# Optimization experiments

Hardware: AMD Instinct MI355X
Metric: run time of the kernel (lower is better)

Reference implementation:

```python
import jax, jax.numpy as jnp
import numpy as np

ALPHA = 1.0
K = 5          # kernel height == width
STRIDE = 1


def extract_patches(x, k, stride):
    """x: (N, C, H, W) -> (N, k*k*C, Ho, Wo), feature order (kh, kw, c)
    to match k.view(kh*kw*C, F) flattening of a (kh, kw, C, F) kernel."""
    p = jax.lax.conv_general_dilated_patches(x, (k, k), (stride, stride), 'VALID')
    N, _, Ho, Wo = p.shape
    C = x.shape[1]
    # conv_general_dilated_patches is channel-major: (C, kh, kw) -> reorder to (kh, kw, C)
    p = p.reshape(N, C, k, k, Ho, Wo).transpose(0, 2, 3, 1, 4, 5)
    return p.reshape(N, k * k * C, Ho, Wo)


def setup_inputs():
    key = jax.random.key(0)
    kx, kk1, kk2 = jax.random.split(key, 3)
    N, C, H, W = 8, 4, 64, 64
    F = 16
    # xavier-uniform-ish scale for kernels
    limit = float(np.sqrt(6.0 / (K * K * C + F)))
    x = jax.random.normal(kx, (N, C, H, W), jnp.float32)
    k1 = jax.random.uniform(kk1, (K, K, C, F), jnp.float32, -limit, limit)
    k2 = jax.random.uniform(kk2, (K, K, C, F), jnp.float32, -limit, limit)
    bias = jnp.zeros((F,), jnp.float32)
    return {"x": x, "k1": k1, "k2": k2, "bias": bias}


def _smooth_max(patches, kflat):
    # patches: (N, P, Ho, Wo); kflat: (P, F)
    z = patches[:, :, None] + kflat[None, :, :, None, None]  # (N, P, F, Ho, Wo)
    w = jax.nn.softmax(ALPHA * z, axis=1)  # exp(alpha*z)/sum over patch dim (stable)
    return jnp.sum(z * w, axis=1)          # (N, F, Ho, Wo)


def reference(x, k1, k2, bias):
    kh, kw, C, F = k1.shape
    patches = extract_patches(x, kh, STRIDE)        # (N, kh*kw*C, Ho, Wo)
    y11 = _smooth_max(patches, k1.reshape(-1, F))   # smooth-max of  x + k1
    y21 = _smooth_max(-patches, k2.reshape(-1, F))  # smooth-max of -x + k2
    return y11 + y21 + bias[None, :, None, None]
```

## Files before the change

### kernel.cpp

```cpp
#include <hip/hip_runtime.h>

#define NN 8
#define CC 4
#define HH 64
#define WW 64
#define KK 5
#define FF 16
#define HO 60
#define WO 60
#define PP (KK * KK * CC)

typedef float v4f __attribute__((ext_vector_type(4)));

#define PQ_ELEMS (CC * KK * 64)
#define LDS_TOT 1536

__global__ void smorph_weights(const float* __restrict__ k1,
                               const float* __restrict__ k2,
                               float* __restrict__ wq) {
    int i = blockIdx.x * blockDim.x + threadIdx.x;
    if (i < 4 * PP * 16) {
        int idx16 = i >> 4;
        int ff = idx16 / PP;
        int p = idx16 - ff * PP;
        int j = i & 15;
        int grp = j >> 2;
        int fi = j & 3;
        int f = ff * 4 + fi;
        const float* kp = (grp >> 1) ? k2 : k1;
        float kv = kp[p * FF + f];
        float e = __expf(kv);
        wq[i] = (grp & 1) ? kv * e : e;
    }
}

__global__ __launch_bounds__(512) void smorph_conv(
        const float* __restrict__ x, const float* __restrict__ wq,
        const float* __restrict__ bias, float* __restrict__ out) {
    __shared__ v4f lds[LDS_TOT];
    v4f* pq = lds;

    int b = blockIdx.x;
    int n = b / (HO * 2);
    int rem = b - n * (HO * 2);
    int ho = rem >> 1;
    int fgh = rem & 1;
    int t = threadIdx.x;

    for (int i = t; i < PQ_ELEMS; i += 512) {
        int w = i & 63;
        int cr = i >> 6;
        int c = cr / KK, r = cr - c * KK;
        float v = x[((n * CC + c) * HH + (ho + r)) * WW + w];
        float e1 = __expf(v), e2 = __expf(-v);
        pq[i] = (v4f){e1, v * e1, e2, -v * e2};
    }
    __syncthreads();

    int lane = t & 63;
    int wid = t >> 6;
    int cw = wid & 3;
    int fgl = wid >> 2;

    int wbi = __builtin_amdgcn_readfirstlane(((fgh * 2 + fgl) * PP + cw) * 16);
    const float* wb = wq + wbi;

    float d1[4] = {0.f, 0.f, 0.f, 0.f}, n1[4] = {0.f, 0.f, 0.f, 0.f};
    float d2[4] = {0.f, 0.f, 0.f, 0.f}, n2[4] = {0.f, 0.f, 0.f, 0.f};

    const v4f* pbase = pq + (cw * KK) * 64 + lane;

#pragma unroll 1
    for (int kh = 0; kh < KK; ++kh) {
        const v4f* prow = pbase + kh * 64;
        v4f q[KK];
#pragma unroll
        for (int kw = 0; kw < KK; ++kw) q[kw] = prow[kw];
#pragma unroll
        for (int kw = 0; kw < KK; ++kw) {
            const float* wp = wb + (kh * KK + kw) * (CC * 16);
            v4f qv = q[kw];
#pragma unroll
            for (int j = 0; j < 4; ++j) {
                float ea1 = wp[j], ba1 = wp[4 + j];
                float ea2 = wp[8 + j], bb2 = wp[12 + j];
                d1[j] = fmaf(qv.x, ea1, d1[j]);
                n1[j] = fmaf(qv.y, ea1, n1[j]);
                n1[j] = fmaf(qv.x, ba1, n1[j]);
                d2[j] = fmaf(qv.z, ea2, d2[j]);
                n2[j] = fmaf(qv.w, ea2, n2[j]);
                n2[j] = fmaf(qv.z, bb2, n2[j]);
            }
        }
    }

    v4f* red = lds;
    __syncthreads();
    if (cw) {
        v4f* rr = red + (((cw - 1) * 2 + fgl) * 4) * 64 + lane;
        rr[0 * 64] = (v4f){d1[0], d1[1], d1[2], d1[3]};
        rr[1 * 64] = (v4f){n1[0], n1[1], n1[2], n1[3]};
        rr[2 * 64] = (v4f){d2[0], d2[1], d2[2], d2[3]};
        rr[3 * 64] = (v4f){n2[0], n2[1], n2[2], n2[3]};
    }
    __syncthreads();
    if (!cw && lane < WO) {
#pragma unroll
        for (int rcw = 0; rcw < 3; ++rcw) {
            const v4f* rr = red + ((rcw * 2 + fgl) * 4) * 64 + lane;
            v4f t0 = rr[0 * 64], t1 = rr[1 * 64];
            v4f t2 = rr[2 * 64], t3 = rr[3 * 64];
#pragma unroll
            for (int j = 0; j < 4; ++j) {
                d1[j] += t0[j]; n1[j] += t1[j];
                d2[j] += t2[j]; n2[j] += t3[j];
            }
        }
        int f0 = (fgh * 2 + fgl) * 4;
#pragma unroll
        for (int j = 0; j < 4; ++j) {
            float o = n1[j] / d1[j] + n2[j] / d2[j] + bias[f0 + j];
            out[((size_t)(n * FF + f0 + j) * HO + ho) * WO + lane] = o;
        }
    }
}

extern "C" void kernel_launch(void* const* d_in, const int* in_sizes, int n_in,
                              void* d_out, int out_size, void* d_ws, size_t ws_size,
                              hipStream_t stream) {
    const float* x    = (const float*)d_in[0];
    const float* k1   = (const float*)d_in[1];
    const float* k2   = (const float*)d_in[2];
    const float* bias = (const float*)d_in[3];
    float* out = (float*)d_out;
    float* wq = (float*)d_ws;

    smorph_weights<<<(4 * PP * 16 + 255) / 256, 256, 0, stream>>>(k1, k2, wq);
    smorph_conv<<<NN * HO * 2, 512, 0, stream>>>(x, wq, bias, out);
}
```

Before: 70.90 us.

## Compute two output rows per block with 2 filters per wave, reusing weight registers

Each block now handles two output rows and a quarter of the filters (2 per wave) instead of one row and half the filters. Weights are reordered so each wave loads 40 contiguous scalars per kernel row into registers and reuses them for both output rows. Input rows are carried across kh iterations in registers (sliding window). The goal is fewer redundant weight loads and less repeated exp work on shared input rows per output; the cost is more registers per thread and an unchanged block count (8*30*4 = 960).

```diff
diff --git a/kernel.cpp b/kernel.cpp
--- a/kernel.cpp
+++ b/kernel.cpp
@@ -10,23 +10,28 @@
 #define WO 60
 #define PP (KK * KK * CC)
 
+#define RPB 2
+#define HPB (HO / RPB)
+#define RIN (RPB + KK - 1)
+
 typedef float v4f __attribute__((ext_vector_type(4)));
 
-#define PQ_ELEMS (CC * KK * 64)
-#define LDS_TOT 1536
+#define PQ_ELEMS (CC * RIN * 64)
+#define LDS_TOT (PQ_ELEMS + 4)
 
 __global__ void smorph_weights(const float* __restrict__ k1,
                                const float* __restrict__ k2,
                                float* __restrict__ wq) {
     int i = blockIdx.x * blockDim.x + threadIdx.x;
-    if (i < 4 * PP * 16) {
-        int idx16 = i >> 4;
-        int ff = idx16 / PP;
-        int p = idx16 - ff * PP;
-        int j = i & 15;
-        int grp = j >> 2;
-        int fi = j & 3;
-        int f = ff * 4 + fi;
+    if (i < 6400) {
+        int rec = i >> 3, j = i & 7;
+        int cfp = rec / 25, khkw = rec - cfp * 25;
+        int kh = khkw / 5, kw = khkw - kh * 5;
+        int fqfp = cfp >> 2, c = cfp & 3;
+        int fq = fqfp >> 1, fp = fqfp & 1;
+        int ff = j & 1, grp = j >> 1;
+        int f = fq * 4 + fp * 2 + ff;
+        int p = (kh * KK + kw) * CC + c;
         const float* kp = (grp >> 1) ? k2 : k1;
         float kv = kp[p * FF + f];
         float e = __expf(kv);
@@ -41,17 +46,18 @@
     v4f* pq = lds;
 
     int b = blockIdx.x;
-    int n = b / (HO * 2);
-    int rem = b - n * (HO * 2);
-    int ho = rem >> 1;
-    int fgh = rem & 1;
+    int n = b / (HPB * 4);
+    int rem = b - n * (HPB * 4);
+    int hp = rem >> 2;
+    int fq = rem & 3;
+    int ho0 = hp * RPB;
     int t = threadIdx.x;
 
     for (int i = t; i < PQ_ELEMS; i += 512) {
         int w = i & 63;
         int cr = i >> 6;
-        int c = cr / KK, r = cr - c * KK;
-        float v = x[((n * CC + c) * HH + (ho + r)) * WW + w];
+        int c = cr / RIN, r = cr - c * RIN;
+        float v = x[((n * CC + c) * HH + (ho0 + r)) * WW + w];
         float e1 = __expf(v), e2 = __expf(-v);
         pq[i] = (v4f){e1, v * e1, e2, -v * e2};
     }
@@ -60,68 +66,89 @@
     int lane = t & 63;
     int wid = t >> 6;
     int cw = wid & 3;
-    int fgl = wid >> 2;
+    int fp = wid >> 2;
 
-    int wbi = __builtin_amdgcn_readfirstlane(((fgh * 2 + fgl) * PP + cw) * 16);
-    const float* wb = wq + wbi;
+    int wbo = __builtin_amdgcn_readfirstlane(((fq * 2 + fp) * CC + cw) * 200);
+    const float* wb = wq + wbo;
 
-    float d1[4] = {0.f, 0.f, 0.f, 0.f}, n1[4] = {0.f, 0.f, 0.f, 0.f};
-    float d2[4] = {0.f, 0.f, 0.f, 0.f}, n2[4] = {0.f, 0.f, 0.f, 0.f};
+    float d1[RPB][2], n1[RPB][2], d2[RPB][2], n2[RPB][2];
+#pragma unroll
+    for (int r = 0; r < RPB; ++r)
+#pragma unroll
+        for (int ff = 0; ff < 2; ++ff) {
+            d1[r][ff] = 0.f; n1[r][ff] = 0.f;
+            d2[r][ff] = 0.f; n2[r][ff] = 0.f;
+        }
 
-    const v4f* pbase = pq + (cw * KK) * 64 + lane;
+    const v4f* pbase = pq + (cw * RIN) * 64 + lane;
+
+    v4f qprev[KK];
+#pragma unroll
+    for (int kw = 0; kw < KK; ++kw) qprev[kw] = pbase[kw];
 
 #pragma unroll 1
     for (int kh = 0; kh < KK; ++kh) {
-        const v4f* prow = pbase + kh * 64;
-        v4f q[KK];
+        const float* wk = wb + kh * 40;
+        float wv[40];
 #pragma unroll
-        for (int kw = 0; kw < KK; ++kw) q[kw] = prow[kw];
+        for (int j = 0; j < 40; ++j) wv[j] = wk[j];
+        const v4f* prow = pbase + (kh + 1) * 64;
+        v4f qn[KK];
+#pragma unroll
+        for (int kw = 0; kw < KK; ++kw) qn[kw] = prow[kw];
 #pragma unroll
         for (int kw = 0; kw < KK; ++kw) {
-            const float* wp = wb + (kh * KK + kw) * (CC * 16);
-            v4f qv = q[kw];
+            v4f q = qprev[kw], qq = qn[kw];
 #pragma unroll
-            for (int j = 0; j < 4; ++j) {
-                float ea1 = wp[j], ba1 = wp[4 + j];
-                float ea2 = wp[8 + j], bb2 = wp[12 + j];
-                d1[j] = fmaf(qv.x, ea1, d1[j]);
-                n1[j] = fmaf(qv.y, ea1, n1[j]);
-                n1[j] = fmaf(qv.x, ba1, n1[j]);
-                d2[j] = fmaf(qv.z, ea2, d2[j]);
-                n2[j] = fmaf(qv.w, ea2, n2[j]);
-                n2[j] = fmaf(qv.z, bb2, n2[j]);
+            for (int ff = 0; ff < 2; ++ff) {
+                float eA1 = wv[kw * 8 + ff],     bA1 = wv[kw * 8 + 2 + ff];
+                float eA2 = wv[kw * 8 + 4 + ff], bA2 = wv[kw * 8 + 6 + ff];
+                d1[0][ff] = fmaf(q.x, eA1, d1[0][ff]);
+                n1[0][ff] = fmaf(q.y, eA1, n1[0][ff]);
+                n1[0][ff] = fmaf(q.x, bA1, n1[0][ff]);
+                d2[0][ff] = fmaf(q.z, eA2, d2[0][ff]);
+                n2[0][ff] = fmaf(q.w, eA2, n2[0][ff]);
+                n2[0][ff] = fmaf(q.z, bA2, n2[0][ff]);
+                d1[1][ff] = fmaf(qq.x, eA1, d1[1][ff]);
+                n1[1][ff] = fmaf(qq.y, eA1, n1[1][ff]);
+                n1[1][ff] = fmaf(qq.x, bA1, n1[1][ff]);
+                d2[1][ff] = fmaf(qq.z, eA2, d2[1][ff]);
+                n2[1][ff] = fmaf(qq.w, eA2, n2[1][ff]);
+                n2[1][ff] = fmaf(qq.z, bA2, n2[1][ff]);
             }
+            qprev[kw] = qn[kw];
         }
     }
 
     v4f* red = lds;
     __syncthreads();
     if (cw) {
-        v4f* rr = red + (((cw - 1) * 2 + fgl) * 4) * 64 + lane;
-        rr[0 * 64] = (v4f){d1[0], d1[1], d1[2], d1[3]};
-        rr[1 * 64] = (v4f){n1[0], n1[1], n1[2], n1[3]};
-        rr[2 * 64] = (v4f){d2[0], d2[1], d2[2], d2[3]};
-        rr[3 * 64] = (v4f){n2[0], n2[1], n2[2], n2[3]};
+        v4f* rr = red + (((cw - 1) * 2 + fp) * 4) * 64 + lane;
+        rr[0 * 64] = (v4f){d1[0][0], d1[0][1], d1[1][0], d1[1][1]};
+        rr[1 * 64] = (v4f){n1[0][0], n1[0][1], n1[1][0], n1[1][1]};
+        rr[2 * 64] = (v4f){d2[0][0], d2[0][1], d2[1][0], d2[1][1]};
+        rr[3 * 64] = (v4f){n2[0][0], n2[0][1], n2[1][0], n2[1][1]};
     }
     __syncthreads();
     if (!cw && lane < WO) {
 #pragma unroll
         for (int rcw = 0; rcw < 3; ++rcw) {
-            const v4f* rr = red + ((rcw * 2 + fgl) * 4) * 64 + lane;
+            const v4f* rr = red + ((rcw * 2 + fp) * 4) * 64 + lane;
             v4f t0 = rr[0 * 64], t1 = rr[1 * 64];
             v4f t2 = rr[2 * 64], t3 = rr[3 * 64];
+            d1[0][0] += t0.x; d1[0][1] += t0.y; d1[1][0] += t0.z; d1[1][1] += t0.w;
+            n1[0][0] += t1.x; n1[0][1] += t1.y; n1[1][0] += t1.z; n1[1][1] += t1.w;
+            d2[0][0] += t2.x; d2[0][1] += t2.y; d2[1][0] += t2.z; d2[1][1] += t2.w;
+            n2[0][0] += t3.x; n2[0][1] += t3.y; n2[1][0] += t3.z; n2[1][1] += t3.w;
+        }
 #pragma unroll
-            for (int j = 0; j < 4; ++j) {
-                d1[j] += t0[j]; n1[j] += t1[j];
-                d2[j] += t2[j]; n2[j] += t3[j];
+        for (int r = 0; r < RPB; ++r)
+#pragma unroll
+            for (int ff = 0; ff < 2; ++ff) {
+                int f = fq * 4 + fp * 2 + ff;
+                float o = n1[r][ff] / d1[r][ff] + n2[r][ff] / d2[r][ff] + bias[f];
+                out[((size_t)(n * FF + f) * HO + (ho0 + r)) * WO + lane] = o;
             }
-        }
-        int f0 = (fgh * 2 + fgl) * 4;
-#pragma unroll
-        for (int j = 0; j < 4; ++j) {
-            float o = n1[j] / d1[j] + n2[j] / d2[j] + bias[f0 + j];
-            out[((size_t)(n * FF + f0 + j) * HO + ho) * WO + lane] = o;
-        }
     }
 }
 
@@ -135,6 +162,6 @@
     float* out = (float*)d_out;
     float* wq = (float*)d_ws;
 
-    smorph_weights<<<(4 * PP * 16 + 255) / 256, 256, 0, stream>>>(k1, k2, wq);
-    smorph_conv<<<NN * HO * 2, 512, 0, stream>>>(x, wq, bias, out);
+    smorph_weights<<<25, 256, 0, stream>>>(k1, k2, wq);
+    smorph_conv<<<NN * HPB * 4, 512, 0, stream>>>(x, wq, bias, out);
 }
```

Result: no change. 72.30 us (+2.0%).
